# Kernel tuning notes

Hardware: AMD Instinct MI355X
Metric: run time of the kernel (lower is better)

Reference implementation:

```python
import jax, jax.numpy as jnp
import numpy as np

LAYERS, BLOCKS = 10, 4
RC, DC, SC, EC = 32, 32, 256, 256  # residual, dilation, skip, end channels
CIN, COUT, K = 6, 1, 2
DILATIONS = [2 ** (i % LAYERS) for i in range(BLOCKS * LAYERS)]
NL = len(DILATIONS)


def conv1d(x, w, dilation=1, pad=0):
    # x: [N, C, T], w: [O, I, K]
    return jax.lax.conv_general_dilated(
        x, w, window_strides=(1,), padding=[(pad, pad)],
        rhs_dilation=(dilation,), dimension_numbers=('NCH', 'OIH', 'NCH'))


def setup_inputs() -> dict:
    key = jax.random.key(0)
    ks = jax.random.split(key, 10)
    s = 0.1
    return {
        'x': jax.random.normal(ks[0], (8, CIN, 8192), dtype=jnp.float32),
        'start_w': jax.random.normal(ks[1], (RC, CIN, 1), dtype=jnp.float32) * s,
        'filter_w': jax.random.normal(ks[2], (NL, DC, RC, K), dtype=jnp.float32) * s,
        'gate_w': jax.random.normal(ks[3], (NL, DC, RC, K), dtype=jnp.float32) * s,
        'res_w': jax.random.normal(ks[4], (NL, RC, DC, 1), dtype=jnp.float32) * s,
        'skip_w': jax.random.normal(ks[5], (NL, SC, DC, 1), dtype=jnp.float32) * s,
        'end1_w': jax.random.normal(ks[6], (EC, SC, 1), dtype=jnp.float32) * s,
        'end1_b': jax.random.normal(ks[7], (EC,), dtype=jnp.float32) * s,
        'end2_w': jax.random.normal(ks[8], (COUT, EC, 1), dtype=jnp.float32) * s,
        'end2_b': jax.random.normal(ks[9], (COUT,), dtype=jnp.float32) * s,
    }


def reference(x, start_w, filter_w, gate_w, res_w, skip_w, end1_w, end1_b, end2_w, end2_b):
    x = conv1d(x, start_w)  # [B, RC, T]
    T = x.shape[2]
    # symmetric padding=(K-1)*d makes length grow by d each layer;
    # the shortest skip is the first one: T + (K-1)*DILATIONS[0]
    min_len = T + (K - 1) * DILATIONS[0]
    skip_sum = jnp.zeros((x.shape[0], SC, min_len), dtype=x.dtype)
    for i, d in enumerate(DILATIONS):
        pad = (K - 1) * d
        f = jnp.tanh(conv1d(x, filter_w[i], d, pad))
        g = jax.nn.sigmoid(conv1d(x, gate_w[i], d, pad))
        x = f * g  # [B, DC, T'] with T' = T_prev + d
        s = conv1d(x, skip_w[i])
        skip_sum = skip_sum + s[:, :, -min_len:]
        x = conv1d(x, res_w[i]) + x  # residual add (RC == DC)
    h = jax.nn.relu(skip_sum)
    h = jax.nn.relu(conv1d(h, end1_w) + end1_b[None, :, None])
    h = conv1d(h, end2_w) + end2_b[None, :, None]
    return h[:, :, -1]  # [B, COUT]
```

## Files before the change

### kernel.cpp

```cpp
#include <hip/hip_runtime.h>
#include <hip/hip_fp16.h>
#include <math.h>


#define NL 40
#define TLEN 8192

#define F_BLOB 0
#define F_C0   40960
#define F_Z    41216
#define F_H    51456
#define F_OB   53504
#define F_CNT  53512

typedef __attribute__((ext_vector_type(2))) _Float16 h2;

#if defined(__has_builtin)
#if __has_builtin(__builtin_amdgcn_fdot2)
#define HAS_FDOT2 1
#endif
#endif

__device__ __forceinline__ float FDOT2(h2 a, h2 b, float c) {
#ifdef HAS_FDOT2
    return __builtin_amdgcn_fdot2(a, b, c, false);
#else
    return c + (float)a.x * (float)b.x + (float)a.y * (float)b.y;
#endif
}

__device__ __forceinline__ float tanh_fast(float f) {
    f = fminf(fmaxf(f, -15.f), 15.f);
    float e2 = __expf(2.f * f);
    return (e2 - 1.f) / (e2 + 1.f);
}

__global__ __launch_bounds__(256) void k1_fold(
    const float* __restrict__ x, const float* __restrict__ start_w,
    const float* __restrict__ filter_w, const float* __restrict__ gate_w,
    const float* __restrict__ res_w, float* __restrict__ ws)
{
    const int l = blockIdx.x, m = blockIdx.y;
    const int t = threadIdx.x;

    if (l == NL) {
        if (m == 0) {
            const int b = t >> 5, ch = t & 31;
            float acc = 0.f;
#pragma unroll
            for (int j = 0; j < 6; ++j)
                acc += start_w[ch * 6 + j] * x[(b * 6 + j) * TLEN + TLEN - 1];
            ws[F_C0 + t] = acc;
            if (t < 8) { ws[F_OB + t] = 0.f; ((int*)(ws + F_CNT))[t] = 0; }
        } else {
            for (int k = t; k < 2048; k += 256) ws[F_H + k] = 0.f;
        }
        return;
    }

    __shared__ float F[32][32];
    __shared__ __align__(16) float R[32][36];
    const float* src = m ? gate_w : filter_w;
    for (int e = t; e < 1024; e += 256)
        F[e >> 5][e & 31] = src[(l * 1024 + e) * 2];
    if (l > 0)
        for (int e = t; e < 1024; e += 256) {
            const int k = e >> 5, j = e & 31;
            R[k][j] = res_w[(l - 1) * 1024 + e] + (k == j ? 1.f : 0.f);
        }
    __syncthreads();

    const int ch = t >> 3, jg = t & 7, j0 = jg * 4;
    float o0, o1, o2, o3;
    if (l == 0) {
        o0 = F[ch][j0]; o1 = F[ch][j0+1]; o2 = F[ch][j0+2]; o3 = F[ch][j0+3];
    } else {
        o0 = o1 = o2 = o3 = 0.f;
#pragma unroll
        for (int k = 0; k < 32; ++k) {
            const float fv = F[ch][k];
            const float4 rv = *(const float4*)&R[k][j0];
            o0 += fv * rv.x; o1 += fv * rv.y; o2 += fv * rv.z; o3 += fv * rv.w;
        }
    }
    const int hh = jg >> 2;
    __half* dst = (__half*)ws + (size_t)l * 2048 + (hh * 32 + ch) * 32
                + (m ? 16 : 0) + (j0 & 15);
    ((__half2*)dst)[0] = __floats2half2_rn(o0, o1);
    ((__half2*)dst)[1] = __floats2half2_rn(o2, o3);
}

#define K2_PREF(L, W) do {                                                   \
    if ((L) < NL) {                                                          \
        _Pragma("unroll")                                                    \
        for (int i = 0; i < 4; ++i)                                          \
            W[i] = blob[(L) * 256 + lane * 4 + i];                           \
    }                                                                        \
} while (0)

#define K2_STEP(L, W) do {                                                   \
    h2 s[8];                                                                 \
    { const float4* sp = (const float4*)zsm;                                 \
      *(float4*)&s[0] = sp[h * 2];                                           \
      *(float4*)&s[4] = sp[h * 2 + 1]; }                                     \
    float f = 0.f, g = 0.f;                                                  \
    const h2* wf = (const h2*)&W[0];                                         \
    const h2* wg = (const h2*)&W[2];                                         \
    _Pragma("unroll")                                                        \
    for (int i = 0; i < 8; ++i) {                                            \
        f = FDOT2(wf[i], s[i], f);                                           \
        g = FDOT2(wg[i], s[i], g);                                           \
    }                                                                        \
    f += __shfl_xor(f, 32, 64);                                              \
    g += __shfl_xor(g, 32, 64);                                              \
    float z = tanh_fast(f) * (1.f / (1.f + __expf(-g)));                     \
    if (h == 0) {                                                            \
        zbuf[((L) * 8 + b) * 32 + ch] = z;                                   \
        zsm[ch] = __float2half(z);                                           \
    }                                                                        \
    __builtin_amdgcn_wave_barrier();                                         \
    K2_PREF((L) + 4, W);                                                     \
} while (0)

__global__ __launch_bounds__(64) void k2_recur(float* __restrict__ ws)
{
    const int b = blockIdx.x;
    const int lane = threadIdx.x;
    const int ch = lane & 31, h = lane >> 5;
    __shared__ __align__(16) __half zsm[32];
    float* zbuf = ws + F_Z;

    if (h == 0) zsm[ch] = __float2half(ws[F_C0 + b * 32 + ch]);
    __builtin_amdgcn_wave_barrier();

    const float4* blob = (const float4*)ws;
    float4 w0[4], w1[4], w2[4], w3[4];
    K2_PREF(0, w0); K2_PREF(1, w1); K2_PREF(2, w2); K2_PREF(3, w3);
    for (int l = 0; l < NL; l += 4) {
        K2_STEP(l + 0, w0);
        K2_STEP(l + 1, w1);
        K2_STEP(l + 2, w2);
        K2_STEP(l + 3, w3);
    }
}

__global__ __launch_bounds__(256) void k3a_skip(
    const float* __restrict__ skip_w, float* __restrict__ ws)
{
    const int l = blockIdx.x, b = blockIdx.y, t = threadIdx.x;
    __shared__ __align__(16) float zsm[32];
    if (t < 32) zsm[t] = ws[F_Z + (l * 8 + b) * 32 + t];
    __syncthreads();
    const float4* w4 = (const float4*)(skip_w + (size_t)(l * 256 + t) * 32);
    const float4* z4 = (const float4*)zsm;
    float acc = 0.f;
#pragma unroll
    for (int i = 0; i < 8; ++i) {
        float4 wv = w4[i], zv = z4[i];
        acc += wv.x*zv.x + wv.y*zv.y + wv.z*zv.z + wv.w*zv.w;
    }
    atomicAdd(&ws[F_H + b * 256 + t], acc);
}

__global__ __launch_bounds__(256) void k3b_end(
    const float* __restrict__ end1_w, const float* __restrict__ end1_b,
    const float* __restrict__ end2_w, const float* __restrict__ end2_b,
    float* __restrict__ ws, float* __restrict__ out)
{
    const int q = blockIdx.x, b = blockIdx.y, t = threadIdx.x;
    __shared__ __align__(16) float hsm[256];
    __shared__ float psum[64][5];
    const int p = t >> 6, oc = t & 63, row = q * 64 + oc;

    float4 wreg[16];
    const float4* wp = (const float4*)(end1_w + (size_t)row * 256 + p * 64);
#pragma unroll
    for (int i = 0; i < 16; ++i) wreg[i] = wp[i];

    hsm[t] = fmaxf(ws[F_H + b * 256 + t], 0.f);
    __syncthreads();
    const float4* h4 = (const float4*)(hsm + p * 64);
    float acc = 0.f;
#pragma unroll
    for (int i = 0; i < 16; ++i) {
        float4 wv = wreg[i], hv = h4[i];
        acc += wv.x*hv.x + wv.y*hv.y + wv.z*hv.z + wv.w*hv.w;
    }
    psum[oc][p] = acc;
    __syncthreads();
    if (t < 64) {
        const int rr = q * 64 + t;
        float e = psum[t][0] + psum[t][1] + psum[t][2] + psum[t][3]
                + end1_b[rr];
        e = fmaxf(e, 0.f);
        float pe = e * end2_w[rr];
#pragma unroll
        for (int off = 32; off > 0; off >>= 1)
            pe += __shfl_down(pe, off, 64);
        if (t == 0) {
            float* obuf = ws + F_OB;
            int* cnt = (int*)(ws + F_CNT);
            atomicAdd(&obuf[b], pe);
            __threadfence();
            int old = __hip_atomic_fetch_add(&cnt[b], 1, __ATOMIC_ACQ_REL,
                                             __HIP_MEMORY_SCOPE_AGENT);
            if (old == 3) {
                float tot = __hip_atomic_load(&obuf[b], __ATOMIC_ACQUIRE,
                                              __HIP_MEMORY_SCOPE_AGENT);
                out[b] = tot + end2_b[0];
            }
        }
    }
}

extern "C" void kernel_launch(void* const* d_in, const int* in_sizes, int n_in,
                              void* d_out, int out_size, void* d_ws, size_t ws_size,
                              hipStream_t stream) {
    const float* x        = (const float*)d_in[0];
    const float* start_w  = (const float*)d_in[1];
    const float* filter_w = (const float*)d_in[2];
    const float* gate_w   = (const float*)d_in[3];
    const float* res_w    = (const float*)d_in[4];
    const float* skip_w   = (const float*)d_in[5];
    const float* end1_w   = (const float*)d_in[6];
    const float* end1_b   = (const float*)d_in[7];
    const float* end2_w   = (const float*)d_in[8];
    const float* end2_b   = (const float*)d_in[9];
    float* out = (float*)d_out;
    float* ws  = (float*)d_ws;

    k1_fold <<<dim3(NL + 1, 2), 256, 0, stream>>>(x, start_w, filter_w,
                                                  gate_w, res_w, ws);
    k2_recur<<<8, 64, 0, stream>>>(ws);
    k3a_skip<<<dim3(NL, 8), 256, 0, stream>>>(skip_w, ws);
    k3b_end <<<dim3(4, 8), 256, 0, stream>>>(end1_w, end1_b, end2_w, end2_b,
                                             ws, out);
}
```

Baseline: 98.54 us.

## Fuse skip accumulation and end convolutions into one per-batch tail kernel

Replaces the skip-sum kernel and the end-projection kernel with a single kernel using one block per batch. That block sums all 40 layers' skip contributions in registers and computes end1, end2 and the output directly. This removes one launch, the atomics, the workspace zeroing and the cross-block completion counter. In exchange it uses only 8 blocks, and each thread streams 40 skip rows plus a 256-wide end1 row serially, so parallelism drops sharply.

```diff
diff --git a/kernel.cpp b/kernel.cpp
--- a/kernel.cpp
+++ b/kernel.cpp
@@ -9,9 +9,6 @@
 #define F_BLOB 0
 #define F_C0   40960
 #define F_Z    41216
-#define F_H    51456
-#define F_OB   53504
-#define F_CNT  53512
 
 typedef __attribute__((ext_vector_type(2))) _Float16 h2;
 
@@ -51,9 +48,6 @@
             for (int j = 0; j < 6; ++j)
                 acc += start_w[ch * 6 + j] * x[(b * 6 + j) * TLEN + TLEN - 1];
             ws[F_C0 + t] = acc;
-            if (t < 8) { ws[F_OB + t] = 0.f; ((int*)(ws + F_CNT))[t] = 0; }
-        } else {
-            for (int k = t; k < 2048; k += 256) ws[F_H + k] = 0.f;
         }
         return;
     }
@@ -144,73 +138,55 @@
     }
 }
 
-__global__ __launch_bounds__(256) void k3a_skip(
-    const float* __restrict__ skip_w, float* __restrict__ ws)
-{
-    const int l = blockIdx.x, b = blockIdx.y, t = threadIdx.x;
-    __shared__ __align__(16) float zsm[32];
-    if (t < 32) zsm[t] = ws[F_Z + (l * 8 + b) * 32 + t];
-    __syncthreads();
-    const float4* w4 = (const float4*)(skip_w + (size_t)(l * 256 + t) * 32);
-    const float4* z4 = (const float4*)zsm;
-    float acc = 0.f;
-#pragma unroll
-    for (int i = 0; i < 8; ++i) {
-        float4 wv = w4[i], zv = z4[i];
-        acc += wv.x*zv.x + wv.y*zv.y + wv.z*zv.z + wv.w*zv.w;
-    }
-    atomicAdd(&ws[F_H + b * 256 + t], acc);
-}
-
-__global__ __launch_bounds__(256) void k3b_end(
+__global__ __launch_bounds__(256) void k3_tail(
+    const float* __restrict__ skip_w,
     const float* __restrict__ end1_w, const float* __restrict__ end1_b,
     const float* __restrict__ end2_w, const float* __restrict__ end2_b,
     float* __restrict__ ws, float* __restrict__ out)
 {
-    const int q = blockIdx.x, b = blockIdx.y, t = threadIdx.x;
+    const int b = blockIdx.x, t = threadIdx.x;
+    __shared__ __align__(16) float zsm[NL * 32];
     __shared__ __align__(16) float hsm[256];
-    __shared__ float psum[64][5];
-    const int p = t >> 6, oc = t & 63, row = q * 64 + oc;
-
-    float4 wreg[16];
-    const float4* wp = (const float4*)(end1_w + (size_t)row * 256 + p * 64);
-#pragma unroll
-    for (int i = 0; i < 16; ++i) wreg[i] = wp[i];
-
-    hsm[t] = fmaxf(ws[F_H + b * 256 + t], 0.f);
-    __syncthreads();
-    const float4* h4 = (const float4*)(hsm + p * 64);
+    __shared__ float psum[4];
+
+    for (int idx = t; idx < NL * 32; idx += 256) {
+        const int l = idx >> 5, ch = idx & 31;
+        zsm[idx] = ws[F_Z + (l * 8 + b) * 32 + ch];
+    }
+    __syncthreads();
+
     float acc = 0.f;
-#pragma unroll
-    for (int i = 0; i < 16; ++i) {
-        float4 wv = wreg[i], hv = h4[i];
-        acc += wv.x*hv.x + wv.y*hv.y + wv.z*hv.z + wv.w*hv.w;
-    }
-    psum[oc][p] = acc;
-    __syncthreads();
-    if (t < 64) {
-        const int rr = q * 64 + t;
-        float e = psum[t][0] + psum[t][1] + psum[t][2] + psum[t][3]
-                + end1_b[rr];
-        e = fmaxf(e, 0.f);
-        float pe = e * end2_w[rr];
-#pragma unroll
-        for (int off = 32; off > 0; off >>= 1)
-            pe += __shfl_down(pe, off, 64);
-        if (t == 0) {
-            float* obuf = ws + F_OB;
-            int* cnt = (int*)(ws + F_CNT);
-            atomicAdd(&obuf[b], pe);
-            __threadfence();
-            int old = __hip_atomic_fetch_add(&cnt[b], 1, __ATOMIC_ACQ_REL,
-                                             __HIP_MEMORY_SCOPE_AGENT);
-            if (old == 3) {
-                float tot = __hip_atomic_load(&obuf[b], __ATOMIC_ACQUIRE,
-                                              __HIP_MEMORY_SCOPE_AGENT);
-                out[b] = tot + end2_b[0];
-            }
-        }
-    }
+    const float4* z4 = (const float4*)zsm;
+#pragma unroll 4
+    for (int l = 0; l < NL; ++l) {
+        const float4* w4 = (const float4*)(skip_w + (size_t)(l * 256 + t) * 32);
+        const float4* zz = z4 + l * 8;
+#pragma unroll
+        for (int i = 0; i < 8; ++i) {
+            float4 wv = w4[i], zv = zz[i];
+            acc += wv.x*zv.x + wv.y*zv.y + wv.z*zv.z + wv.w*zv.w;
+        }
+    }
+    hsm[t] = fmaxf(acc, 0.f);
+    __syncthreads();
+
+    float e = 0.f;
+    const float4* w1 = (const float4*)(end1_w + (size_t)t * 256);
+    const float4* h4 = (const float4*)hsm;
+#pragma unroll
+    for (int i = 0; i < 64; ++i) {
+        float4 wv = w1[i], hv = h4[i];
+        e += wv.x*hv.x + wv.y*hv.y + wv.z*hv.z + wv.w*hv.w;
+    }
+    e = fmaxf(e + end1_b[t], 0.f);
+    float pe = e * end2_w[t];
+#pragma unroll
+    for (int off = 32; off > 0; off >>= 1)
+        pe += __shfl_down(pe, off, 64);
+    if ((t & 63) == 0) psum[t >> 6] = pe;
+    __syncthreads();
+    if (t == 0)
+        out[b] = psum[0] + psum[1] + psum[2] + psum[3] + end2_b[0];
 }
 
 extern "C" void kernel_launch(void* const* d_in, const int* in_sizes, int n_in,
@@ -232,7 +208,6 @@
     k1_fold <<<dim3(NL + 1, 2), 256, 0, stream>>>(x, start_w, filter_w,
                                                   gate_w, res_w, ws);
     k2_recur<<<8, 64, 0, stream>>>(ws);
-    k3a_skip<<<dim3(NL, 8), 256, 0, stream>>>(skip_w, ws);
-    k3b_end <<<dim3(4, 8), 256, 0, stream>>>(end1_w, end1_b, end2_w, end2_b,
-                                             ws, out);
-}
+    k3_tail <<<8, 256, 0, stream>>>(skip_w, end1_w, end1_b, end2_w, end2_b,
+                                    ws, out);
+}
```

New measurement: 144.2 us. 1.46x slower.

## Fuse skip projection into recurrence kernel, overlapping with gated layer steps

Applied to the files above, without the earlier changes.

Merges the recurrence kernel and the skip-projection kernel into one 320-thread block per batch. One wave runs the serial gated-layer recurrence and keeps z history in shared memory, while four other waves compute the skip projection for the previous four layers in a pipelined way. Accumulation happens in registers, so atomics, the zero-init of the skip buffer and the global z buffer are no longer needed, and the relu moves into this kernel. This removes one kernel launch and the global round trip, but adds block-wide barriers into the serial recurrence loop, and only 8 blocks do the skip work.

```diff
diff --git a/kernel.cpp b/kernel.cpp
--- a/kernel.cpp
+++ b/kernel.cpp
@@ -8,7 +8,6 @@
 
 #define F_BLOB 0
 #define F_C0   40960
-#define F_Z    41216
 #define F_H    51456
 #define F_OB   53504
 #define F_CNT  53512
@@ -52,8 +51,6 @@
                 acc += start_w[ch * 6 + j] * x[(b * 6 + j) * TLEN + TLEN - 1];
             ws[F_C0 + t] = acc;
             if (t < 8) { ws[F_OB + t] = 0.f; ((int*)(ws + F_CNT))[t] = 0; }
-        } else {
-            for (int k = t; k < 2048; k += 256) ws[F_H + k] = 0.f;
         }
         return;
     }
@@ -99,67 +96,90 @@
 } while (0)
 
 #define K2_STEP(L, W) do {                                                   \
-    h2 s[8];                                                                 \
+    h2 sv[8];                                                                \
     { const float4* sp = (const float4*)zsm;                                 \
-      *(float4*)&s[0] = sp[h * 2];                                           \
-      *(float4*)&s[4] = sp[h * 2 + 1]; }                                     \
+      *(float4*)&sv[0] = sp[h * 2];                                          \
+      *(float4*)&sv[4] = sp[h * 2 + 1]; }                                    \
     float f = 0.f, g = 0.f;                                                  \
     const h2* wf = (const h2*)&W[0];                                         \
     const h2* wg = (const h2*)&W[2];                                         \
     _Pragma("unroll")                                                        \
     for (int i = 0; i < 8; ++i) {                                            \
-        f = FDOT2(wf[i], s[i], f);                                           \
-        g = FDOT2(wg[i], s[i], g);                                           \
+        f = FDOT2(wf[i], sv[i], f);                                          \
+        g = FDOT2(wg[i], sv[i], g);                                          \
     }                                                                        \
     f += __shfl_xor(f, 32, 64);                                              \
     g += __shfl_xor(g, 32, 64);                                              \
     float z = tanh_fast(f) * (1.f / (1.f + __expf(-g)));                     \
     if (h == 0) {                                                            \
-        zbuf[((L) * 8 + b) * 32 + ch] = z;                                   \
+        zhist[(L) * 32 + ch] = z;                                            \
         zsm[ch] = __float2half(z);                                           \
     }                                                                        \
     __builtin_amdgcn_wave_barrier();                                         \
     K2_PREF((L) + 4, W);                                                     \
 } while (0)
 
-__global__ __launch_bounds__(64) void k2_recur(float* __restrict__ ws)
+__global__ __launch_bounds__(320) void k2_all(
+    const float* __restrict__ skip_w, float* __restrict__ ws)
 {
-    const int b = blockIdx.x;
-    const int lane = threadIdx.x;
-    const int ch = lane & 31, h = lane >> 5;
+    const int b = blockIdx.x, t = threadIdx.x;
     __shared__ __align__(16) __half zsm[32];
-    float* zbuf = ws + F_Z;
-
-    if (h == 0) zsm[ch] = __float2half(ws[F_C0 + b * 32 + ch]);
-    __builtin_amdgcn_wave_barrier();
-
+    __shared__ __align__(16) float zhist[NL * 32];
+
+    const int lane = t, ch = t & 31, h = (t >> 5) & 1;
+    const int s = t - 64;
     const float4* blob = (const float4*)ws;
     float4 w0[4], w1[4], w2[4], w3[4];
-    K2_PREF(0, w0); K2_PREF(1, w1); K2_PREF(2, w2); K2_PREF(3, w3);
-    for (int l = 0; l < NL; l += 4) {
-        K2_STEP(l + 0, w0);
-        K2_STEP(l + 1, w1);
-        K2_STEP(l + 2, w2);
-        K2_STEP(l + 3, w3);
-    }
-}
-
-__global__ __launch_bounds__(256) void k3a_skip(
-    const float* __restrict__ skip_w, float* __restrict__ ws)
-{
-    const int l = blockIdx.x, b = blockIdx.y, t = threadIdx.x;
-    __shared__ __align__(16) float zsm[32];
-    if (t < 32) zsm[t] = ws[F_Z + (l * 8 + b) * 32 + t];
-    __syncthreads();
-    const float4* w4 = (const float4*)(skip_w + (size_t)(l * 256 + t) * 32);
-    const float4* z4 = (const float4*)zsm;
-    float acc = 0.f;
-#pragma unroll
-    for (int i = 0; i < 8; ++i) {
-        float4 wv = w4[i], zv = z4[i];
-        acc += wv.x*zv.x + wv.y*zv.y + wv.z*zv.z + wv.w*zv.w;
-    }
-    atomicAdd(&ws[F_H + b * 256 + t], acc);
+    float a0 = 0.f, a1 = 0.f, a2 = 0.f, a3 = 0.f;
+
+    if (t < 64) {
+        if (h == 0) zsm[ch] = __float2half(ws[F_C0 + b * 32 + ch]);
+        K2_PREF(0, w0); K2_PREF(1, w1); K2_PREF(2, w2); K2_PREF(3, w3);
+    }
+    __syncthreads();
+
+    for (int p = 0; p < 10; ++p) {
+        if (t < 64) {
+            const int l0 = p * 4;
+            K2_STEP(l0 + 0, w0);
+            K2_STEP(l0 + 1, w1);
+            K2_STEP(l0 + 2, w2);
+            K2_STEP(l0 + 3, w3);
+        } else if (p > 0) {
+            const int lb = (p - 1) * 4;
+#pragma unroll
+            for (int dl = 0; dl < 4; ++dl) {
+                const int l = lb + dl;
+                const float4* w4 =
+                    (const float4*)(skip_w + ((size_t)l * 256 + s) * 32);
+                const float4* z4 = (const float4*)(zhist + l * 32);
+#pragma unroll
+                for (int i = 0; i < 8; ++i) {
+                    float4 wv = w4[i], zv = z4[i];
+                    a0 += wv.x * zv.x; a1 += wv.y * zv.y;
+                    a2 += wv.z * zv.z; a3 += wv.w * zv.w;
+                }
+            }
+        }
+        __syncthreads();
+    }
+
+    if (t >= 64) {
+#pragma unroll
+        for (int dl = 0; dl < 4; ++dl) {
+            const int l = 36 + dl;
+            const float4* w4 =
+                (const float4*)(skip_w + ((size_t)l * 256 + s) * 32);
+            const float4* z4 = (const float4*)(zhist + l * 32);
+#pragma unroll
+            for (int i = 0; i < 8; ++i) {
+                float4 wv = w4[i], zv = z4[i];
+                a0 += wv.x * zv.x; a1 += wv.y * zv.y;
+                a2 += wv.z * zv.z; a3 += wv.w * zv.w;
+            }
+        }
+        ws[F_H + b * 256 + s] = fmaxf((a0 + a1) + (a2 + a3), 0.f);
+    }
 }
 
 __global__ __launch_bounds__(256) void k3b_end(
@@ -177,7 +197,7 @@
 #pragma unroll
     for (int i = 0; i < 16; ++i) wreg[i] = wp[i];
 
-    hsm[t] = fmaxf(ws[F_H + b * 256 + t], 0.f);
+    hsm[t] = ws[F_H + b * 256 + t];
     __syncthreads();
     const float4* h4 = (const float4*)(hsm + p * 64);
     float acc = 0.f;
@@ -231,8 +251,7 @@
 
     k1_fold <<<dim3(NL + 1, 2), 256, 0, stream>>>(x, start_w, filter_w,
                                                   gate_w, res_w, ws);
-    k2_recur<<<8, 64, 0, stream>>>(ws);
-    k3a_skip<<<dim3(NL, 8), 256, 0, stream>>>(skip_w, ws);
+    k2_all  <<<8, 320, 0, stream>>>(skip_w, ws);
     k3b_end <<<dim3(4, 8), 256, 0, stream>>>(end1_w, end1_b, end2_w, end2_b,
                                              ws, out);
 }
```

Measured after the change: 133.7 us. 35.7% more time.

## Prefetch later-stage weights into L2 during recurrence and use shuffles for state

Applied to the files above, without the earlier changes.

The recurrence kernel now launches extra blocks that only touch the skip and end-layer weights, warming L2 so the following kernels find them cached. The dummy conditional store keeps those loads from being removed. The recurrent state exchange also moves from LDS with wave barriers to register shuffles that pack pairs of halves. This adds extra blocks and memory traffic running alongside a latency-bound serial kernel.

```diff
diff --git a/kernel.cpp b/kernel.cpp
--- a/kernel.cpp
+++ b/kernel.cpp
@@ -12,6 +12,7 @@
 #define F_H    51456
 #define F_OB   53504
 #define F_CNT  53512
+#define F_DUMP 60000
 
 typedef __attribute__((ext_vector_type(2))) _Float16 h2;
 
@@ -99,39 +100,57 @@
 } while (0)
 
 #define K2_STEP(L, W) do {                                                   \
-    h2 s[8];                                                                 \
-    { const float4* sp = (const float4*)zsm;                                 \
-      *(float4*)&s[0] = sp[h * 2];                                           \
-      *(float4*)&s[4] = sp[h * 2 + 1]; }                                     \
+         \
+    float zx = __shfl_xor(z, 1, 64);                                         \
+    float ze = (ch & 1) ? zx : z;                                            \
+    float zo = (ch & 1) ? z  : zx;                                           \
+    __half2 pk = __halves2half2(__float2half(ze), __float2half(zo));         \
+    int pki; __builtin_memcpy(&pki, &pk, 4);                                 \
+    h2 sv[8];                                                                \
+    _Pragma("unroll")                                                        \
+    for (int i = 0; i < 8; ++i) {                                            \
+        int q = __shfl(pki, hbase + 2 * i, 64);                              \
+        __builtin_memcpy(&sv[i], &q, 4);                                     \
+    }                                                                        \
     float f = 0.f, g = 0.f;                                                  \
     const h2* wf = (const h2*)&W[0];                                         \
     const h2* wg = (const h2*)&W[2];                                         \
     _Pragma("unroll")                                                        \
     for (int i = 0; i < 8; ++i) {                                            \
-        f = FDOT2(wf[i], s[i], f);                                           \
-        g = FDOT2(wg[i], s[i], g);                                           \
+        f = FDOT2(wf[i], sv[i], f);                                          \
+        g = FDOT2(wg[i], sv[i], g);                                          \
     }                                                                        \
     f += __shfl_xor(f, 32, 64);                                              \
     g += __shfl_xor(g, 32, 64);                                              \
-    float z = tanh_fast(f) * (1.f / (1.f + __expf(-g)));                     \
-    if (h == 0) {                                                            \
-        zbuf[((L) * 8 + b) * 32 + ch] = z;                                   \
-        zsm[ch] = __float2half(z);                                           \
-    }                                                                        \
-    __builtin_amdgcn_wave_barrier();                                         \
+    z = tanh_fast(f) * (1.f / (1.f + __expf(-g)));                           \
+    if (h == 0) zbuf[((L) * 8 + b) * 32 + ch] = z;                           \
     K2_PREF((L) + 4, W);                                                     \
 } while (0)
 
-__global__ __launch_bounds__(64) void k2_recur(float* __restrict__ ws)
-{
-    const int b = blockIdx.x;
-    const int lane = threadIdx.x;
-    const int ch = lane & 31, h = lane >> 5;
-    __shared__ __align__(16) __half zsm[32];
+__global__ __launch_bounds__(256) void k2_recur(
+    const float* __restrict__ skip_w, const float* __restrict__ end1_w,
+    const float* __restrict__ end1_b, const float* __restrict__ end2_w,
+    float* __restrict__ ws)
+{
+    const int bi = blockIdx.x, t = threadIdx.x;
+
+    if (bi >= 8) {
+        const int wi = (bi - 8) * 256 + t;
+        const float4* s4 = (const float4*)skip_w;
+        const float4* e4 = (const float4*)end1_w;
+        float acc = 0.f;
+        for (int i = wi; i < 81920; i += 32768) acc += s4[i].x;
+        if (wi < 16384) acc += e4[wi].x;
+        if (wi < 64) acc += end2_w[wi * 4] + end1_b[wi * 4];
+        if (acc == 1234.567f) ws[F_DUMP] = acc;
+        return;
+    }
+    if (t >= 64) return;
+
+    const int b = bi, lane = t;
+    const int ch = lane & 31, h = lane >> 5, hbase = h << 4;
     float* zbuf = ws + F_Z;
-
-    if (h == 0) zsm[ch] = __float2half(ws[F_C0 + b * 32 + ch]);
-    __builtin_amdgcn_wave_barrier();
+    float z = ws[F_C0 + b * 32 + ch];
 
     const float4* blob = (const float4*)ws;
     float4 w0[4], w1[4], w2[4], w3[4];
@@ -231,7 +250,7 @@
 
     k1_fold <<<dim3(NL + 1, 2), 256, 0, stream>>>(x, start_w, filter_w,
                                                   gate_w, res_w, ws);
-    k2_recur<<<8, 64, 0, stream>>>(ws);
+    k2_recur<<<136, 256, 0, stream>>>(skip_w, end1_w, end1_b, end2_w, ws);
     k3a_skip<<<dim3(NL, 8), 256, 0, stream>>>(skip_w, ws);
     k3b_end <<<dim3(4, 8), 256, 0, stream>>>(end1_w, end1_b, end2_w, end2_b,
                                              ws, out);
```

After: 98.44 us. No clear change (-0.1%).
